# Kernel tuning notes

Measured on AMD Instinct MI355X. Metric: run time of the kernel, lower is better.

The kernel has to match this reference:

```python
import jax, jax.numpy as jnp
import numpy as np

DIM = 1024
HEADS = 16
HEAD_DIM = DIM // HEADS
B, S, L0, L1 = 2, 2048, 2048, 2048


def setup_inputs() -> dict:
    key = jax.random.key(0)
    ks = jax.random.split(key, 10)
    sc = DIM ** -0.5
    return {
        "query": jax.random.normal(ks[0], (B, S, DIM), jnp.float32),
        "l0_keys": jax.random.normal(ks[1], (B, L0, DIM), jnp.float32),
        "l0_values": jax.random.normal(ks[2], (B, L0, DIM), jnp.float32),
        "l1_keys": jax.random.normal(ks[3], (B, L1, DIM), jnp.float32),
        "l1_values": jax.random.normal(ks[4], (B, L1, DIM), jnp.float32),
        "l0_mask": jax.random.randint(ks[5], (S, L0), 0, 2, jnp.int32),
        "Wq": jax.random.normal(ks[6], (DIM, DIM), jnp.float32) * sc,
        "bq": jnp.zeros((DIM,), jnp.float32),
        "Wo": jax.random.normal(ks[7], (DIM, DIM), jnp.float32) * sc,
        "bo": jnp.zeros((DIM,), jnp.float32),
        "gate": jnp.asarray(0.0, jnp.float32),
    }


def reference(query, l0_keys, l0_values, l1_keys, l1_values, l0_mask, Wq, bq, Wo, bo, gate):
    b, s, d = query.shape
    h, hd = HEADS, HEAD_DIM
    scale = hd ** -0.5
    # q: [B,H,S,hd]
    q = (query @ Wq.T + bq).reshape(b, s, h, hd).transpose(0, 2, 1, 3)

    def attend(keys, values, mask):
        L = keys.shape[1]
        k = keys.reshape(b, L, h, hd)
        v = values.reshape(b, L, h, hd)
        scores = jnp.einsum("bhsd,blhd->bhsl", q, k) * scale
        if mask is not None:
            scores = jnp.where(mask[None, None] == 0, -jnp.inf, scores)
        w = jax.nn.softmax(scores, axis=-1)  # [B,H,S,L]
        out = jnp.einsum("bhsl,blhd->bshd", w, v)  # [B,S,H,hd]
        return out, w.mean(axis=1)

    out0, a0 = attend(l0_keys, l0_values, l0_mask)
    out1, a1 = attend(l1_keys, l1_values, None)
    g = jax.nn.sigmoid(gate)
    out = (g * out0 + (1.0 - g) * out1).reshape(b, s, d)
    out = out @ Wo.T + bo
    return out, a0, a1
```

## Files before the change

kernel.cpp:

```cpp
#include <hip/hip_runtime.h>

#define DIM   1024
#define HEADS 16
#define HD    64
#define BB    2
#define SS    2048
#define LLL   2048
#define LOG2E 1.4426950408889634f

typedef __bf16 bf16x8 __attribute__((ext_vector_type(8)));
typedef __bf16 bf16x4v __attribute__((ext_vector_type(4)));
typedef float  f32x4  __attribute__((ext_vector_type(4)));
typedef short  s16x4  __attribute__((ext_vector_type(4)));
typedef short  s16x8  __attribute__((ext_vector_type(8)));
typedef unsigned short u16;

static __device__ __forceinline__ u16 f2b(float x) {
  unsigned u = __float_as_uint(x);
  u += 0x7fffu + ((u >> 16) & 1u);
  return (u16)(u >> 16);
}
static __device__ __forceinline__ float b2f(u16 u) {
  return __uint_as_float(((unsigned)u) << 16);
}
static __device__ __forceinline__ f32x4 mfma32(bf16x8 a, bf16x8 b, f32x4 c) {
  return __builtin_amdgcn_mfma_f32_16x16x32_bf16(a, b, c, 0, 0, 0);
}
static __device__ __forceinline__ f32x4 mfma16(s16x4 a, s16x4 b, f32x4 c) {
#if __has_builtin(__builtin_amdgcn_mfma_f32_16x16x16bf16_1k)
  return __builtin_amdgcn_mfma_f32_16x16x16bf16_1k(a, b, c, 0, 0, 0);
#else
  asm volatile("v_mfma_f32_16x16x16_bf16 %0, %1, %2, %0" : "+v"(c) : "v"(a), "v"(b));
  return c;
#endif
}

static __device__ __forceinline__ void gload_lds16(const void* g, void* lds_uniform_base) {
#if __has_builtin(__builtin_amdgcn_global_load_lds)
  __builtin_amdgcn_global_load_lds(
      (const __attribute__((address_space(1))) unsigned int*)g,
      (__attribute__((address_space(3))) unsigned int*)lds_uniform_base, 16, 0, 0);
#else
  const int l = threadIdx.x & 63;
  ((uint4*)lds_uniform_base)[l] = ((const uint4*)g)[0];
#endif
}

__global__ void cvt_f32_bf16(const float* __restrict__ src, u16* __restrict__ dst, int n4) {
  int i = blockIdx.x * blockDim.x + threadIdx.x;
  if (i >= n4) return;
  float4 f = ((const float4*)src)[i];
  ushort4 o;
  o.x = f2b(f.x); o.y = f2b(f.y); o.z = f2b(f.z); o.w = f2b(f.w);
  ((ushort4*)dst)[i] = o;
}

__global__ void mask_pack(const int* __restrict__ mask, unsigned* __restrict__ mbits) {
  int i = blockIdx.x * blockDim.x + threadIdx.x;
  const int* src = mask + (size_t)i * 32;
  unsigned bm = 0;
#pragma unroll
  for (int j = 0; j < 8; ++j) {
    int4 m = ((const int4*)src)[j];
    bm |= (m.x != 0 ? 1u : 0u) << (j * 4 + 0);
    bm |= (m.y != 0 ? 1u : 0u) << (j * 4 + 1);
    bm |= (m.z != 0 ? 1u : 0u) << (j * 4 + 2);
    bm |= (m.w != 0 ? 1u : 0u) << (j * 4 + 3);
  }
  mbits[i] = bm;
}

__global__ __launch_bounds__(256) void pack_k(const float* __restrict__ k0,
                                              const float* __restrict__ k1,
                                              u16* __restrict__ Kfrag) {
  const float SCK = 0.125f * LOG2E;
  const int w = threadIdx.x >> 6, l = threadIdx.x & 63, g = l >> 4, li = l & 15;
  const int lt = blockIdx.x * 4 + w, h = blockIdx.y, z = blockIdx.z;
  const int lay = z >> 1, b = z & 1;
  const float* src = (lay ? k1 : k0) + (size_t)b * LLL * DIM;
  u16* dst = Kfrag + ((((size_t)z * HEADS + h) * 32 + lt) * 8) * 512;
#pragma unroll
  for (int c = 0; c < 8; ++c) {
    int mt = c >> 1, kk = c & 1;
    const float* p = &src[(size_t)(lt * 64 + mt * 16 + li) * DIM + h * 64 + kk * 32 + g * 8];
    float4 f0 = *(const float4*)p;
    float4 f1 = *(const float4*)(p + 4);
    u16 u[8] = {f2b(f0.x * SCK), f2b(f0.y * SCK), f2b(f0.z * SCK), f2b(f0.w * SCK),
                f2b(f1.x * SCK), f2b(f1.y * SCK), f2b(f1.z * SCK), f2b(f1.w * SCK)};
    *(uint4*)&dst[c * 512 + l * 8] = *(uint4*)u;
  }
}

__global__ __launch_bounds__(256) void pack_v(const float* __restrict__ v0,
                                              const float* __restrict__ v1,
                                              u16* __restrict__ Vfrag) {
  __shared__ u16 T[64][72];
  const int lt = blockIdx.x, h = blockIdx.y, z = blockIdx.z;
  const int lay = z >> 1, b = z & 1;
  const float* v = (lay ? v1 : v0) + (size_t)b * LLL * DIM;
  const int t = threadIdx.x;
  {
    int r = t >> 2, c16 = (t & 3) * 16;
    const float* src = &v[(size_t)(lt * 64 + r) * DIM + h * 64 + c16];
#pragma unroll
    for (int i = 0; i < 4; ++i) {
      float4 f = *(const float4*)&src[i * 4];
      T[r][c16 + i * 4 + 0] = f2b(f.x);
      T[r][c16 + i * 4 + 1] = f2b(f.y);
      T[r][c16 + i * 4 + 2] = f2b(f.z);
      T[r][c16 + i * 4 + 3] = f2b(f.w);
    }
  }
  __syncthreads();
  u16* dst = Vfrag + ((((size_t)z * HEADS + h) * 32 + lt) * 8) * 512;
  {
    int lane = t & 63, g = lane >> 4, li = lane & 15;
#pragma unroll
    for (int cc = 0; cc < 2; ++cc) {
      int c = (t >> 6) + cc * 4;
      int mt = c >> 1, p = c & 1;
      u16 u[8];
#pragma unroll
      for (int j = 0; j < 4; ++j) u[j] = T[mt * 16 + 4 * g + j][p * 32 + li];
#pragma unroll
      for (int j = 0; j < 4; ++j) u[4 + j] = T[mt * 16 + 4 * g + j][p * 32 + 16 + li];
      *(uint4*)&dst[c * 512 + lane * 8] = *(uint4*)u;
    }
  }
}

template<int MODE>
__global__ __launch_bounds__(256) void gemm_nt(const u16* __restrict__ A,
                                               const u16* __restrict__ Bt,
                                               const float* __restrict__ bias,
                                               void* __restrict__ Cv,
                                               int M, int N, int K) {
  __shared__ u16 As[128][64];
  __shared__ u16 Bs[64][64];
  const int t = threadIdx.x;
  const int w = t >> 6, l = t & 63, g = l >> 4, li = l & 15;
  const int m0 = blockIdx.y * 128, n0 = blockIdx.x * 64;
  const int slotL = w * 64 + l;
  const int rA = slotL >> 3, cA = ((slotL & 7) * 8) ^ ((rA & 7) * 8);
  f32x4 acc[2][4] = {};
  for (int kt = 0; kt < K; kt += 64) {
#pragma unroll
    for (int s = 0; s < 4; ++s) {
      int r = rA + s * 32;
      gload_lds16(&A[(size_t)(m0 + r) * K + kt + cA], &As[0][0] + (s * 256 + w * 64) * 8);
    }
#pragma unroll
    for (int s = 0; s < 2; ++s) {
      int r = rA + s * 32;
      gload_lds16(&Bt[(size_t)(n0 + r) * K + kt + cA], &Bs[0][0] + (s * 256 + w * 64) * 8);
    }
    __syncthreads();
#pragma unroll
    for (int kk = 0; kk < 2; ++kk) {
      bf16x8 a[2], bfr[4];
#pragma unroll
      for (int mi = 0; mi < 2; ++mi) {
        int ra = w * 32 + mi * 16 + li;
        a[mi] = *(const bf16x8*)&As[ra][(kk * 32 + g * 8) ^ ((ra & 7) << 3)];
      }
#pragma unroll
      for (int ni = 0; ni < 4; ++ni) {
        int rb = ni * 16 + li;
        bfr[ni] = *(const bf16x8*)&Bs[rb][(kk * 32 + g * 8) ^ ((rb & 7) << 3)];
      }
#pragma unroll
      for (int mi = 0; mi < 2; ++mi)
#pragma unroll
        for (int ni = 0; ni < 4; ++ni)
          acc[mi][ni] = mfma32(a[mi], bfr[ni], acc[mi][ni]);
    }
    __syncthreads();
  }
#pragma unroll
  for (int mi = 0; mi < 2; ++mi)
#pragma unroll
    for (int ni = 0; ni < 4; ++ni)
#pragma unroll
      for (int v = 0; v < 4; ++v) {
        int rr = m0 + w * 32 + mi * 16 + g * 4 + v;
        int cc = n0 + ni * 16 + li;
        float val = acc[mi][ni][v] + bias[cc];
        if (MODE == 1) {
          ((float*)Cv)[(size_t)rr * N + cc] = val;
        } else {
          int b = rr >> 11, q = rr & 2047;
          int qt = q >> 5, n = (q >> 4) & 1, liq = q & 15;
          int h = (cc >> 6) & 15, kk2 = (cc >> 5) & 1, gp = (cc >> 3) & 3, j = cc & 7;
          size_t base = ((((size_t)b * HEADS + h) * 64 + qt) * 4 + n * 2 + kk2) * 512;
          ((u16*)Cv)[base + (size_t)(gp * 16 + liq) * 8 + j] = f2b(val);
        }
      }
}

template<int MASKED>
static __device__ __forceinline__ void attn_pv_body(int z, int h, int qt2, int w, int l,
                                                    const u16* __restrict__ Qfrag,
                                                    const u16* __restrict__ Kfrag,
                                                    const u16* __restrict__ Vfrag,
                                                    const unsigned* __restrict__ mbits,
                                                    u16* __restrict__ out01,
                                                    float* __restrict__ db,
                                                    u16* __restrict__ KV) {
  const int g = l >> 4, li = l & 15;
  const int b = z & 1;
  const int qt = qt2 >> 1, n = qt2 & 1;
  const u16* kfh = Kfrag + (size_t)(z * HEADS + h) * (32 * 8 * 512);
  const u16* vfh = Vfrag + (size_t)(z * HEADS + h) * (32 * 8 * 512);
  const u16* qfh = Qfrag + ((((size_t)(b * HEADS + h) * 64 + qt) * 4 + n * 2)) * 512;

  bf16x8 qf0 = *(const bf16x8*)&qfh[0 * 512 + l * 8];
  bf16x8 qf1 = *(const bf16x8*)&qfh[1 * 512 + l * 8];

  const unsigned* mrow = MASKED ? mbits + (size_t)(qt2 * 16 + li) * (LLL / 32) : nullptr;
  const int shb = 4 * g;
  const s16x4 ones = {(short)0x3F80, (short)0x3F80, (short)0x3F80, (short)0x3F80};

  auto stage = [&](int buf, int lt) {
    const u16* kfl = kfh + (size_t)lt * 4096;
    const u16* vfl = vfh + (size_t)lt * 4096;
#pragma unroll
    for (int i2 = 0; i2 < 2; ++i2) {
      int f = w * 2 + i2;
      const u16* gsrc = (f < 8 ? kfl + f * 512 : vfl + (f - 8) * 512) + l * 8;
      gload_lds16(gsrc, (char*)KV + buf * 16384 + f * 1024);
    }
  };

  f32x4 dacc = {};
  f32x4 oacc[4] = {};

  stage(0, 0);
  __syncthreads();
  int cur = 0;
  for (int lt = 0; lt < 32; ++lt) {
    if (lt + 1 < 32) stage(cur ^ 1, lt + 1);
    unsigned mw[2];
    if (MASKED) { mw[0] = mrow[lt * 2]; mw[1] = mrow[lt * 2 + 1]; }
    const u16* Ks = KV + cur * 8192;
    const u16* Vs = Ks + 4096;
#pragma unroll
    for (int mt = 0; mt < 4; ++mt) {
      f32x4 s = {};
      __builtin_amdgcn_s_setprio(1);
      s = mfma32(*(const bf16x8*)&Ks[(mt * 2 + 0) * 512 + l * 8], qf0, s);
      s = mfma32(*(const bf16x8*)&Ks[(mt * 2 + 1) * 512 + l * 8], qf1, s);
      __builtin_amdgcn_s_setprio(0);
      f32x4 ev;
      unsigned mm = MASKED ? (mw[mt >> 1] >> ((mt & 1) * 16 + shb)) : 0u;
#pragma unroll
      for (int v = 0; v < 4; ++v) {
        float e = __builtin_amdgcn_exp2f(s[v]);
        if (MASKED) {
          int spread = ((int)(mm << (31 - v))) >> 31;
          e = __uint_as_float(__float_as_uint(e) & (unsigned)spread);
        }
        ev[v] = e;
      }
      bf16x4v wb = __builtin_convertvector(ev, bf16x4v);
      s16x4 wpk = __builtin_bit_cast(s16x4, wb);
      __builtin_amdgcn_s_setprio(1);
      dacc = mfma16(ones, wpk, dacc);
#pragma unroll
      for (int p = 0; p < 2; ++p) {
        s16x8 vf = *(const s16x8*)&Vs[(mt * 2 + p) * 512 + l * 8];
        s16x4 lo = __builtin_shufflevector(vf, vf, 0, 1, 2, 3);
        s16x4 hi = __builtin_shufflevector(vf, vf, 4, 5, 6, 7);
        oacc[2 * p + 0] = mfma16(lo, wpk, oacc[2 * p + 0]);
        oacc[2 * p + 1] = mfma16(hi, wpk, oacc[2 * p + 1]);
      }
      __builtin_amdgcn_s_setprio(0);
    }
    __syncthreads();
    cur ^= 1;
  }
  float r = dacc[0];
  float dinv = 1.0f / r;
  if (l < 16) db[(size_t)(z * HEADS + h) * SS + qt2 * 16 + li] = -__log2f(r);
  u16* ob = out01 + (size_t)z * SS * DIM;
#pragma unroll
  for (int dt = 0; dt < 4; ++dt) {
    f32x4 o = oacc[dt] * dinv;
    ushort4 us;
    us.x = f2b(o[0]); us.y = f2b(o[1]); us.z = f2b(o[2]); us.w = f2b(o[3]);
    *(ushort4*)&ob[((size_t)(qt2 * 16 + li)) * DIM + h * HD + dt * 16 + 4 * g] = us;
  }
}

__global__ __launch_bounds__(512, 8) void attn_pv(const u16* __restrict__ Qfrag,
                                                  const u16* __restrict__ Kfrag,
                                                  const u16* __restrict__ Vfrag,
                                                  const unsigned* __restrict__ mbits,
                                                  u16* __restrict__ out01,
                                                  float* __restrict__ db) {
  __shared__ u16 KV[2][8192];
  const int flat = blockIdx.x;
  const int xcd = flat & 7, i = flat >> 3;
  const int k = i >> 4, qg = i & 15;
  const int zh = xcd + 8 * k;
  const int z = zh >> 4, h = zh & 15;
  const int w = threadIdx.x >> 6, l = threadIdx.x & 63;
  const int qt2 = qg * 8 + w;
  if (z < 2) attn_pv_body<1>(z, h, qt2, w, l, Qfrag, Kfrag, Vfrag, mbits, out01, db, &KV[0][0]);
  else       attn_pv_body<0>(z, h, qt2, w, l, Qfrag, Kfrag, Vfrag, mbits, out01, db, &KV[0][0]);
}

template<int MASKED>
static __device__ __forceinline__ void amean_body(int z, int qt2, int lt, int w, int l,
                                                  const u16* __restrict__ Qfrag,
                                                  const u16* __restrict__ Kfrag,
                                                  const unsigned* __restrict__ mbits,
                                                  const float* __restrict__ db,
                                                  float* __restrict__ aout,
                                                  u16* __restrict__ KS) {
  const int g = l >> 4, li = l & 15;
  const int b = z & 1;
  const int qt = qt2 >> 1, n = qt2 & 1;

  unsigned mw[2];
  if (MASKED) {
    const unsigned* m0 = mbits + (size_t)(qt2 * 16 + li) * (LLL / 32) + lt * 2;
    mw[0] = m0[0]; mw[1] = m0[1];
  }
  const u16* qf_base = Qfrag + ((((size_t)(b * HEADS) * 64 + qt) * 4 + n * 2)) * 512 + l * 8;
  const float* dbb = db + (size_t)(z * HEADS) * SS + qt2 * 16 + li;

  auto stageK = [&](int buf, int h) {
    const u16* kfh = Kfrag + ((((size_t)(z * HEADS + h)) * 32 + lt) * 8) * 512;
#pragma unroll
    for (int i2 = 0; i2 < 2; ++i2) {
      int f = w * 2 + i2;
      gload_lds16(kfh + f * 512 + l * 8, (char*)KS + buf * 8192 + f * 1024);
    }
  };

  f32x4 asum[4] = {};
  stageK(0, 0);
  __syncthreads();
#pragma unroll 2
  for (int h = 0; h < HEADS; ++h) {
    if (h + 1 < HEADS) stageK((h + 1) & 1, h + 1);
    float l2 = dbb[(size_t)h * SS];
    bf16x8 qf0 = *(const bf16x8*)&qf_base[(size_t)h * (64 * 4 * 512)];
    bf16x8 qf1 = *(const bf16x8*)&qf_base[(size_t)h * (64 * 4 * 512) + 512];
    const u16* Ks = KS + (h & 1) * 4096;
#pragma unroll
    for (int mt = 0; mt < 4; ++mt) {
      f32x4 s = {};
      s = mfma32(*(const bf16x8*)&Ks[(mt * 2 + 0) * 512 + l * 8], qf0, s);
      s = mfma32(*(const bf16x8*)&Ks[(mt * 2 + 1) * 512 + l * 8], qf1, s);
      unsigned mm = MASKED ? (mw[mt >> 1] >> ((mt & 1) * 16 + 4 * g)) : 0u;
#pragma unroll
      for (int v = 0; v < 4; ++v) {
        float e = __builtin_amdgcn_exp2f(s[v] + l2);
        if (MASKED) {
          int spread = ((int)(mm << (31 - v))) >> 31;
          e = __uint_as_float(__float_as_uint(e) & (unsigned)spread);
        }
        asum[mt][v] += e;
      }
    }
    __syncthreads();
  }
  float* ab = aout + (size_t)z * SS * LLL;
#pragma unroll
  for (int mt = 0; mt < 4; ++mt) {
    f32x4 o = asum[mt] * 0.0625f;
    f32x4* dst = (f32x4*)&ab[(size_t)(qt2 * 16 + li) * LLL + lt * 64 + mt * 16 + 4 * g];
    __builtin_nontemporal_store(o, dst);
  }
}

__global__ __launch_bounds__(256, 8) void amean(const u16* __restrict__ Qfrag,
                                                const u16* __restrict__ Kfrag,
                                                const unsigned* __restrict__ mbits,
                                                const float* __restrict__ db,
                                                float* __restrict__ aout) {
  __shared__ u16 KS[2][4096];
  const int flat = blockIdx.x;
  const int xcd = flat & 7, i = flat >> 3;
  const int k = i >> 5, qg = i & 31;
  const int zlt = xcd + 8 * k;
  const int z = zlt >> 5, lt = zlt & 31;
  const int w = threadIdx.x >> 6, l = threadIdx.x & 63;
  const int qt2 = qg * 4 + w;
  if (z < 2) amean_body<1>(z, qt2, lt, w, l, Qfrag, Kfrag, mbits, db, aout, &KS[0][0]);
  else       amean_body<0>(z, qt2, lt, w, l, Qfrag, Kfrag, mbits, db, aout, &KS[0][0]);
}

__global__ void merge_kernel(const u16* __restrict__ o01,
                             const float* __restrict__ gate,
                             u16* __restrict__ merged) {
  int i = blockIdx.x * blockDim.x + threadIdx.x;
  float gv = gate[0];
  float g = 1.0f / (1.0f + __builtin_amdgcn_exp2f(-gv * LOG2E));
  const size_t n = (size_t)BB * SS * DIM;
  ushort4 a = ((const ushort4*)o01)[i];
  ushort4 c = ((const ushort4*)(o01 + n))[i];
  ushort4 o;
  o.x = f2b(g * b2f(a.x) + (1.f - g) * b2f(c.x));
  o.y = f2b(g * b2f(a.y) + (1.f - g) * b2f(c.y));
  o.z = f2b(g * b2f(a.z) + (1.f - g) * b2f(c.z));
  o.w = f2b(g * b2f(a.w) + (1.f - g) * b2f(c.w));
  ((ushort4*)merged)[i] = o;
}

extern "C" void kernel_launch(void* const* d_in, const int* in_sizes, int n_in,
                              void* d_out, int out_size, void* d_ws, size_t ws_size,
                              hipStream_t stream) {
  const float* query = (const float*)d_in[0];
  const float* k0f   = (const float*)d_in[1];
  const float* v0f   = (const float*)d_in[2];
  const float* k1f   = (const float*)d_in[3];
  const float* v1f   = (const float*)d_in[4];
  const int*   mask  = (const int*)d_in[5];
  const float* Wqf   = (const float*)d_in[6];
  const float* bq    = (const float*)d_in[7];
  const float* Wof   = (const float*)d_in[8];
  const float* bo    = (const float*)d_in[9];
  const float* gate  = (const float*)d_in[10];
  float* out = (float*)d_out;

  const size_t nQ = (size_t)BB * SS * DIM;
  const size_t nW = (size_t)DIM * DIM;

  char* ws = (char*)d_ws;
  size_t off = 0;
  auto alloc = [&](size_t bytes) -> char* {
    char* p = ws + off;
    off += (bytes + 255) & ~(size_t)255;
    return p;
  };
  u16*      queryb  = (u16*)alloc(nQ * 2);
  u16*      wqb     = (u16*)alloc(nW * 2);
  u16*      wob     = (u16*)alloc(nW * 2);
  u16*      Qfrag   = (u16*)alloc(nQ * 2);
  u16*      Kfrag   = (u16*)alloc((size_t)2 * nQ * 2);
  u16*      Vfrag   = (u16*)alloc((size_t)2 * nQ * 2);
  unsigned* mbits   = (unsigned*)alloc((size_t)SS * (LLL / 32) * 4);
  float*    db      = (float*)alloc((size_t)4 * HEADS * SS * 4);
  u16*      out01   = (u16*)alloc((size_t)2 * nQ * 2);
  u16*      mergedb = queryb;

  auto cvt = [&](const float* s, u16* d, size_t n) {
    int n4 = (int)(n / 4);
    cvt_f32_bf16<<<dim3((n4 + 255) / 256), dim3(256), 0, stream>>>(s, d, n4);
  };
  cvt(query, queryb, nQ);
  cvt(Wqf, wqb, nW);
  cvt(Wof, wob, nW);

  mask_pack<<<dim3(SS * (LLL / 32) / 256), dim3(256), 0, stream>>>(mask, mbits);
  pack_k<<<dim3(LLL / 64 / 4, HEADS, 4), dim3(256), 0, stream>>>(k0f, k1f, Kfrag);
  pack_v<<<dim3(LLL / 64, HEADS, 4), dim3(256), 0, stream>>>(v0f, v1f, Vfrag);

  gemm_nt<2><<<dim3(DIM / 64, (BB * SS) / 128), dim3(256), 0, stream>>>(
      queryb, wqb, bq, (void*)Qfrag, BB * SS, DIM, DIM);

  attn_pv<<<dim3(1024), dim3(512), 0, stream>>>(Qfrag, Kfrag, Vfrag, mbits, out01, db);

  amean<<<dim3(4096), dim3(256), 0, stream>>>(Qfrag, Kfrag, mbits, db, out + nQ);

  merge_kernel<<<dim3((int)(nQ / 4 / 256)), dim3(256), 0, stream>>>(out01, gate, mergedb);

  gemm_nt<1><<<dim3(DIM / 64, (BB * SS) / 128), dim3(256), 0, stream>>>(
      mergedb, wob, bo, (void*)out, BB * SS, DIM, DIM);
}
```

Measured before the change: 235.7 us.

## Process two 16-row query tiles per wave to reuse K/V fragments

Each wave in attn_pv and amean now handles 32 query rows (two 16-row sub-tiles) instead of 16. Every K and V fragment read from LDS feeds MFMAs for both sub-tiles, which halves LDS reads and global K/V staging per query. Grid sizes are halved and launch bounds drop from 8 to 4 waves per SIMD because register use grows. The cost is lower occupancy and fewer blocks to hide latency.

```diff
diff --git a/kernel.cpp b/kernel.cpp
--- a/kernel.cpp
+++ b/kernel.cpp
@@ -198,7 +198,7 @@
 }
 
 template<int MASKED>
-static __device__ __forceinline__ void attn_pv_body(int z, int h, int qt2, int w, int l,
+static __device__ __forceinline__ void attn_pv_body(int z, int h, int qt, int w, int l,
                                                     const u16* __restrict__ Qfrag,
                                                     const u16* __restrict__ Kfrag,
                                                     const u16* __restrict__ Vfrag,
@@ -208,15 +208,19 @@
                                                     u16* __restrict__ KV) {
   const int g = l >> 4, li = l & 15;
   const int b = z & 1;
-  const int qt = qt2 >> 1, n = qt2 & 1;
   const u16* kfh = Kfrag + (size_t)(z * HEADS + h) * (32 * 8 * 512);
   const u16* vfh = Vfrag + (size_t)(z * HEADS + h) * (32 * 8 * 512);
-  const u16* qfh = Qfrag + ((((size_t)(b * HEADS + h) * 64 + qt) * 4 + n * 2)) * 512;
-
-  bf16x8 qf0 = *(const bf16x8*)&qfh[0 * 512 + l * 8];
-  bf16x8 qf1 = *(const bf16x8*)&qfh[1 * 512 + l * 8];
-
-  const unsigned* mrow = MASKED ? mbits + (size_t)(qt2 * 16 + li) * (LLL / 32) : nullptr;
+  const u16* qfh = Qfrag + (((size_t)(b * HEADS + h) * 64 + qt) * 4) * 512;
+
+  bf16x8 qf[2][2];
+#pragma unroll
+  for (int n = 0; n < 2; ++n)
+#pragma unroll
+    for (int kk = 0; kk < 2; ++kk)
+      qf[n][kk] = *(const bf16x8*)&qfh[(n * 2 + kk) * 512 + l * 8];
+
+  const unsigned* mrow0 = MASKED ? mbits + (size_t)(qt * 32 + li) * (LLL / 32) : nullptr;
+  const unsigned* mrow1 = MASKED ? mrow0 + 16 * (LLL / 32) : nullptr;
   const int shb = 4 * g;
   const s16x4 ones = {(short)0x3F80, (short)0x3F80, (short)0x3F80, (short)0x3F80};
 
@@ -231,67 +235,89 @@
     }
   };
 
-  f32x4 dacc = {};
-  f32x4 oacc[4] = {};
+  f32x4 dacc[2] = {};
+  f32x4 oacc[4][2] = {};
 
   stage(0, 0);
   __syncthreads();
   int cur = 0;
   for (int lt = 0; lt < 32; ++lt) {
     if (lt + 1 < 32) stage(cur ^ 1, lt + 1);
-    unsigned mw[2];
-    if (MASKED) { mw[0] = mrow[lt * 2]; mw[1] = mrow[lt * 2 + 1]; }
+    unsigned mw[2][2];
+    if (MASKED) {
+      mw[0][0] = mrow0[lt * 2]; mw[0][1] = mrow0[lt * 2 + 1];
+      mw[1][0] = mrow1[lt * 2]; mw[1][1] = mrow1[lt * 2 + 1];
+    }
     const u16* Ks = KV + cur * 8192;
     const u16* Vs = Ks + 4096;
 #pragma unroll
     for (int mt = 0; mt < 4; ++mt) {
-      f32x4 s = {};
+      bf16x8 k0 = *(const bf16x8*)&Ks[(mt * 2 + 0) * 512 + l * 8];
+      bf16x8 k1 = *(const bf16x8*)&Ks[(mt * 2 + 1) * 512 + l * 8];
+      f32x4 s[2] = {};
       __builtin_amdgcn_s_setprio(1);
-      s = mfma32(*(const bf16x8*)&Ks[(mt * 2 + 0) * 512 + l * 8], qf0, s);
-      s = mfma32(*(const bf16x8*)&Ks[(mt * 2 + 1) * 512 + l * 8], qf1, s);
+#pragma unroll
+      for (int n = 0; n < 2; ++n) {
+        s[n] = mfma32(k0, qf[n][0], s[n]);
+        s[n] = mfma32(k1, qf[n][1], s[n]);
+      }
       __builtin_amdgcn_s_setprio(0);
-      f32x4 ev;
-      unsigned mm = MASKED ? (mw[mt >> 1] >> ((mt & 1) * 16 + shb)) : 0u;
-#pragma unroll
-      for (int v = 0; v < 4; ++v) {
-        float e = __builtin_amdgcn_exp2f(s[v]);
-        if (MASKED) {
-          int spread = ((int)(mm << (31 - v))) >> 31;
-          e = __uint_as_float(__float_as_uint(e) & (unsigned)spread);
+      s16x4 wpk[2];
+#pragma unroll
+      for (int n = 0; n < 2; ++n) {
+        unsigned mm = MASKED ? (mw[n][mt >> 1] >> ((mt & 1) * 16 + shb)) : 0u;
+        f32x4 ev;
+#pragma unroll
+        for (int v = 0; v < 4; ++v) {
+          float e = __builtin_amdgcn_exp2f(s[n][v]);
+          if (MASKED) {
+            int spread = ((int)(mm << (31 - v))) >> 31;
+            e = __uint_as_float(__float_as_uint(e) & (unsigned)spread);
+          }
+          ev[v] = e;
         }
-        ev[v] = e;
-      }
-      bf16x4v wb = __builtin_convertvector(ev, bf16x4v);
-      s16x4 wpk = __builtin_bit_cast(s16x4, wb);
+        bf16x4v wb = __builtin_convertvector(ev, bf16x4v);
+        wpk[n] = __builtin_bit_cast(s16x4, wb);
+      }
       __builtin_amdgcn_s_setprio(1);
-      dacc = mfma16(ones, wpk, dacc);
+      dacc[0] = mfma16(ones, wpk[0], dacc[0]);
+      dacc[1] = mfma16(ones, wpk[1], dacc[1]);
 #pragma unroll
       for (int p = 0; p < 2; ++p) {
         s16x8 vf = *(const s16x8*)&Vs[(mt * 2 + p) * 512 + l * 8];
         s16x4 lo = __builtin_shufflevector(vf, vf, 0, 1, 2, 3);
         s16x4 hi = __builtin_shufflevector(vf, vf, 4, 5, 6, 7);
-        oacc[2 * p + 0] = mfma16(lo, wpk, oacc[2 * p + 0]);
-        oacc[2 * p + 1] = mfma16(hi, wpk, oacc[2 * p + 1]);
+#pragma unroll
+        for (int n = 0; n < 2; ++n) {
+          oacc[2 * p + 0][n] = mfma16(lo, wpk[n], oacc[2 * p + 0][n]);
+          oacc[2 * p + 1][n] = mfma16(hi, wpk[n], oacc[2 * p + 1][n]);
+        }
       }
       __builtin_amdgcn_s_setprio(0);
     }
     __syncthreads();
     cur ^= 1;
   }
-  float r = dacc[0];
-  float dinv = 1.0f / r;
-  if (l < 16) db[(size_t)(z * HEADS + h) * SS + qt2 * 16 + li] = -__log2f(r);
+  float dinv[2];
+  dinv[0] = 1.0f / dacc[0][0];
+  dinv[1] = 1.0f / dacc[1][0];
+  if (l < 16) {
+    db[(size_t)(z * HEADS + h) * SS + qt * 32 + li]      = -__log2f(dacc[0][0]);
+    db[(size_t)(z * HEADS + h) * SS + qt * 32 + 16 + li] = -__log2f(dacc[1][0]);
+  }
   u16* ob = out01 + (size_t)z * SS * DIM;
 #pragma unroll
-  for (int dt = 0; dt < 4; ++dt) {
-    f32x4 o = oacc[dt] * dinv;
-    ushort4 us;
-    us.x = f2b(o[0]); us.y = f2b(o[1]); us.z = f2b(o[2]); us.w = f2b(o[3]);
-    *(ushort4*)&ob[((size_t)(qt2 * 16 + li)) * DIM + h * HD + dt * 16 + 4 * g] = us;
-  }
-}
-
-__global__ __launch_bounds__(512, 8) void attn_pv(const u16* __restrict__ Qfrag,
+  for (int dt = 0; dt < 4; ++dt)
+#pragma unroll
+    for (int n = 0; n < 2; ++n) {
+      f32x4 o = oacc[dt][n] * dinv[n];
+      ushort4 us;
+      us.x = f2b(o[0]); us.y = f2b(o[1]); us.z = f2b(o[2]); us.w = f2b(o[3]);
+      *(ushort4*)&ob[((size_t)(qt * 32 + n * 16 + li)) * DIM + h * HD + dt * 16 + 4 * g] = us;
+    }
+}
+
+__global__ __launch_bounds__(512, 4) void attn_pv(const u16* __restrict__ Qfrag,
                                                   const u16* __restrict__ Kfrag,
                                                   const u16* __restrict__ Vfrag,
                                                   const unsigned* __restrict__ mbits,
@@ -300,17 +326,17 @@
   __shared__ u16 KV[2][8192];
   const int flat = blockIdx.x;
   const int xcd = flat & 7, i = flat >> 3;
-  const int k = i >> 4, qg = i & 15;
+  const int k = i >> 3, qg = i & 7;
   const int zh = xcd + 8 * k;
   const int z = zh >> 4, h = zh & 15;
   const int w = threadIdx.x >> 6, l = threadIdx.x & 63;
-  const int qt2 = qg * 8 + w;
-  if (z < 2) attn_pv_body<1>(z, h, qt2, w, l, Qfrag, Kfrag, Vfrag, mbits, out01, db, &KV[0][0]);
-  else       attn_pv_body<0>(z, h, qt2, w, l, Qfrag, Kfrag, Vfrag, mbits, out01, db, &KV[0][0]);
+  const int qt = qg * 8 + w;
+  if (z < 2) attn_pv_body<1>(z, h, qt, w, l, Qfrag, Kfrag, Vfrag, mbits, out01, db, &KV[0][0]);
+  else       attn_pv_body<0>(z, h, qt, w, l, Qfrag, Kfrag, Vfrag, mbits, out01, db, &KV[0][0]);
 }
 
 template<int MASKED>
-static __device__ __forceinline__ void amean_body(int z, int qt2, int lt, int w, int l,
+static __device__ __forceinline__ void amean_body(int z, int qt, int lt, int w, int l,
                                                   const u16* __restrict__ Qfrag,
                                                   const u16* __restrict__ Kfrag,
                                                   const unsigned* __restrict__ mbits,
@@ -319,15 +345,16 @@
                                                   u16* __restrict__ KS) {
   const int g = l >> 4, li = l & 15;
   const int b = z & 1;
-  const int qt = qt2 >> 1, n = qt2 & 1;
-
-  unsigned mw[2];
+
+  unsigned mw[2][2];
   if (MASKED) {
-    const unsigned* m0 = mbits + (size_t)(qt2 * 16 + li) * (LLL / 32) + lt * 2;
-    mw[0] = m0[0]; mw[1] = m0[1];
-  }
-  const u16* qf_base = Qfrag + ((((size_t)(b * HEADS) * 64 + qt) * 4 + n * 2)) * 512 + l * 8;
-  const float* dbb = db + (size_t)(z * HEADS) * SS + qt2 * 16 + li;
+    const unsigned* m0 = mbits + (size_t)(qt * 32 + li) * (LLL / 32) + lt * 2;
+    const unsigned* m1 = m0 + 16 * (LLL / 32);
+    mw[0][0] = m0[0]; mw[0][1] = m0[1];
+    mw[1][0] = m1[0]; mw[1][1] = m1[1];
+  }
+  const u16* qf_base = Qfrag + (((size_t)(b * HEADS) * 64 + qt) * 4) * 512 + l * 8;
+  const float* dbb = db + (size_t)(z * HEADS) * SS + qt * 32 + li;
 
   auto stageK = [&](int buf, int h) {
     const u16* kfh = Kfrag + ((((size_t)(z * HEADS + h)) * 32 + lt) * 8) * 512;
@@ -338,44 +365,57 @@
     }
   };
 
-  f32x4 asum[4] = {};
+  f32x4 asum[4][2] = {};
   stageK(0, 0);
   __syncthreads();
 #pragma unroll 2
   for (int h = 0; h < HEADS; ++h) {
     if (h + 1 < HEADS) stageK((h + 1) & 1, h + 1);
-    float l2 = dbb[(size_t)h * SS];
-    bf16x8 qf0 = *(const bf16x8*)&qf_base[(size_t)h * (64 * 4 * 512)];
-    bf16x8 qf1 = *(const bf16x8*)&qf_base[(size_t)h * (64 * 4 * 512) + 512];
+    float l2[2];
+    l2[0] = dbb[(size_t)h * SS];
+    l2[1] = dbb[(size_t)h * SS + 16];
+    bf16x8 qf[2][2];
+#pragma unroll
+    for (int n = 0; n < 2; ++n)
+#pragma unroll
+      for (int kk = 0; kk < 2; ++kk)
+        qf[n][kk] = *(const bf16x8*)&qf_base[(size_t)h * (64 * 4 * 512) + (n * 2 + kk) * 512];
     const u16* Ks = KS + (h & 1) * 4096;
 #pragma unroll
     for (int mt = 0; mt < 4; ++mt) {
-      f32x4 s = {};
-      s = mfma32(*(const bf16x8*)&Ks[(mt * 2 + 0) * 512 + l * 8], qf0, s);
-      s = mfma32(*(const bf16x8*)&Ks[(mt * 2 + 1) * 512 + l * 8], qf1, s);
-      unsigned mm = MASKED ? (mw[mt >> 1] >> ((mt & 1) * 16 + 4 * g)) : 0u;
-#pragma unroll
-      for (int v = 0; v < 4; ++v) {
-        float e = __builtin_amdgcn_exp2f(s[v] + l2);
-        if (MASKED) {
-          int spread = ((int)(mm << (31 - v))) >> 31;
-          e = __uint_as_float(__float_as_uint(e) & (unsigned)spread);
+      bf16x8 k0 = *(const bf16x8*)&Ks[(mt * 2 + 0) * 512 + l * 8];
+      bf16x8 k1 = *(const bf16x8*)&Ks[(mt * 2 + 1) * 512 + l * 8];
+#pragma unroll
+      for (int n = 0; n < 2; ++n) {
+        f32x4 s = {};
+        s = mfma32(k0, qf[n][0], s);
+        s = mfma32(k1, qf[n][1], s);
+        unsigned mm = MASKED ? (mw[n][mt >> 1] >> ((mt & 1) * 16 + 4 * g)) : 0u;
+#pragma unroll
+        for (int v = 0; v < 4; ++v) {
+          float e = __builtin_amdgcn_exp2f(s[v] + l2[n]);
+          if (MASKED) {
+            int spread = ((int)(mm << (31 - v))) >> 31;
+            e = __uint_as_float(__float_as_uint(e) & (unsigned)spread);
+          }
+          asum[mt][n][v] += e;
         }
-        asum[mt][v] += e;
       }
     }
     __syncthreads();
   }
   float* ab = aout + (size_t)z * SS * LLL;
 #pragma unroll
-  for (int mt = 0; mt < 4; ++mt) {
-    f32x4 o = asum[mt] * 0.0625f;
-    f32x4* dst = (f32x4*)&ab[(size_t)(qt2 * 16 + li) * LLL + lt * 64 + mt * 16 + 4 * g];
-    __builtin_nontemporal_store(o, dst);
-  }
-}
-
-__global__ __launch_bounds__(256, 8) void amean(const u16* __restrict__ Qfrag,
+  for (int mt = 0; mt < 4; ++mt)
+#pragma unroll
+    for (int n = 0; n < 2; ++n) {
+      f32x4 o = asum[mt][n] * 0.0625f;
+      f32x4* dst = (f32x4*)&ab[(size_t)(qt * 32 + n * 16 + li) * LLL + lt * 64 + mt * 16 + 4 * g];
+      __builtin_nontemporal_store(o, dst);
+    }
+}
+
+__global__ __launch_bounds__(256, 4) void amean(const u16* __restrict__ Qfrag,
                                                 const u16* __restrict__ Kfrag,
                                                 const unsigned* __restrict__ mbits,
                                                 const float* __restrict__ db,
@@ -383,13 +423,13 @@
   __shared__ u16 KS[2][4096];
   const int flat = blockIdx.x;
   const int xcd = flat & 7, i = flat >> 3;
-  const int k = i >> 5, qg = i & 31;
+  const int k = i >> 4, qg = i & 15;
   const int zlt = xcd + 8 * k;
   const int z = zlt >> 5, lt = zlt & 31;
   const int w = threadIdx.x >> 6, l = threadIdx.x & 63;
-  const int qt2 = qg * 4 + w;
-  if (z < 2) amean_body<1>(z, qt2, lt, w, l, Qfrag, Kfrag, mbits, db, aout, &KS[0][0]);
-  else       amean_body<0>(z, qt2, lt, w, l, Qfrag, Kfrag, mbits, db, aout, &KS[0][0]);
+  const int qt = qg * 4 + w;
+  if (z < 2) amean_body<1>(z, qt, lt, w, l, Qfrag, Kfrag, mbits, db, aout, &KS[0][0]);
+  else       amean_body<0>(z, qt, lt, w, l, Qfrag, Kfrag, mbits, db, aout, &KS[0][0]);
 }
 
 __global__ void merge_kernel(const u16* __restrict__ o01,
@@ -461,9 +501,9 @@
   gemm_nt<2><<<dim3(DIM / 64, (BB * SS) / 128), dim3(256), 0, stream>>>(
       queryb, wqb, bq, (void*)Qfrag, BB * SS, DIM, DIM);
 
-  attn_pv<<<dim3(1024), dim3(512), 0, stream>>>(Qfrag, Kfrag, Vfrag, mbits, out01, db);
-
-  amean<<<dim3(4096), dim3(256), 0, stream>>>(Qfrag, Kfrag, mbits, db, out + nQ);
+  attn_pv<<<dim3(512), dim3(512), 0, stream>>>(Qfrag, Kfrag, Vfrag, mbits, out01, db);
+
+  amean<<<dim3(2048), dim3(256), 0, stream>>>(Qfrag, Kfrag, mbits, db, out + nQ);
 
   merge_kernel<<<dim3((int)(nQ / 4 / 256)), dim3(256), 0, stream>>>(out01, gate, mergedb);
 
```

After: 226.4 us. 1.04x faster.
